# Kernel optimization log

Measured on AMD Instinct MI355X. Metric: run time of the kernel, lower is better.

The kernel has to match this reference:

```python
import jax, jax.numpy as jnp
import numpy as np

NEG = -1e30  # log-space 'zero' (avoid real -inf for stable exp/grad)


def _ctc_loss_mean(logp, targets, target_lengths, blank):
    """CTC loss, PyTorch semantics (reduction='mean', zero_infinity=True).
    logp: (B, T, V) log-probabilities; targets: (B, L) padded labels;
    target_lengths: (B,) ints. All input lengths are T (uniform here).
    """
    B, T, V = logp.shape
    L = targets.shape[1]
    S = 2 * L + 1  # extended label length: blank-interleaved

    ext = jnp.full((B, S), blank, dtype=targets.dtype)
    ext = ext.at[:, 1::2].set(targets)  # blanks at even s, labels at odd s

    s = jnp.arange(S)
    valid = s[None, :] < (2 * target_lengths + 1)[:, None]  # (B, S)
    prev2 = jnp.pad(ext[:, :-2], ((0, 0), (2, 0)), constant_values=blank)
    # skip transition s-2 -> s allowed only at non-blank s with no label repeat
    allow_skip = (s[None, :] >= 2) & (ext != blank) & (ext != prev2)

    # per-(t, s) emission log-prob, masked outside valid extended labels
    emit = jnp.take_along_axis(
        logp, jnp.broadcast_to(ext[:, None, :], (B, T, S)), axis=2
    )  # (B, T, S)
    emit = jnp.where(valid[:, None, :], emit, NEG)

    alpha0 = jnp.full((B, S), NEG, dtype=logp.dtype)
    alpha0 = alpha0.at[:, 0].set(emit[:, 0, 0])
    alpha0 = alpha0.at[:, 1].set(emit[:, 0, 1])

    def step(alpha, e):
        a1 = alpha
        a2 = jnp.pad(alpha[:, :-1], ((0, 0), (1, 0)), constant_values=NEG)
        a3 = jnp.pad(alpha[:, :-2], ((0, 0), (2, 0)), constant_values=NEG)
        a3 = jnp.where(allow_skip, a3, NEG)
        m = jnp.maximum(jnp.maximum(a1, a2), a3)
        new = m + jnp.log(jnp.exp(a1 - m) + jnp.exp(a2 - m) + jnp.exp(a3 - m)) + e
        return new, None

    alpha, _ = jax.lax.scan(step, alpha0, jnp.swapaxes(emit, 0, 1)[1:])

    i1 = (2 * target_lengths).astype(jnp.int32)
    l1 = jnp.take_along_axis(alpha, i1[:, None], axis=1)[:, 0]
    l2 = jnp.take_along_axis(alpha, jnp.maximum(i1 - 1, 0)[:, None], axis=1)[:, 0]
    l2 = jnp.where(target_lengths > 0, l2, NEG)
    m = jnp.maximum(l1, l2)
    loss = -(m + jnp.log(jnp.exp(l1 - m) + jnp.exp(l2 - m)))  # (B,)
    loss = jnp.where(loss > 1e20, 0.0, loss)  # zero_infinity=True
    # reduction='mean': divide by target length, then batch mean
    return jnp.mean(loss / jnp.maximum(target_lengths, 1).astype(loss.dtype))


def setup_inputs() -> dict:
    key = jax.random.key(0)
    kl, kt, kn = jax.random.split(key, 3)
    B, T, V, L = 32, 1024, 1000, 256
    logits = jax.random.normal(kl, (B, T, V), dtype=jnp.float32)
    targets = jax.random.randint(kt, (B, L), 1, V).astype(jnp.int32)
    lengths = jax.random.randint(kn, (B,), L // 2 + 2, L + 1)
    target_padding_mask = jnp.arange(L)[None, :] < lengths[:, None]  # bool (B, L)
    return {"logits": logits, "targets": targets,
            "target_padding_mask": target_padding_mask}


def reference(logits, targets, target_padding_mask):
    blank = 0
    lg = logits[:, :-1, :]            # drop last frame
    tgt = targets[:, 1:]              # drop leading (SOS) token
    logp = jax.nn.log_softmax(lg, axis=-1)  # (B, T-1, V)
    tlen = target_padding_mask.sum(axis=1).astype(jnp.int32) - 1
    return _ctc_loss_mean(logp, tgt, tlen, blank)
```

## Files before the change

### kernel.cpp

```cpp
#include <hip/hip_runtime.h>

#define LOG2E 1.4426950408889634f
#define LN2   0.6931471805599453

static constexpr int B  = 32;
static constexpr int T  = 1024;
static constexpr int TT = 1023;
static constexpr int V  = 1000;
static constexpr int L  = 256;
static constexpr int S  = 511;
static constexpr int SP = 512;
static constexpr int TP = 1024;

using h8  = __attribute__((ext_vector_type(8))) _Float16;

__device__ __forceinline__ float fexp2(float x) {
#if __has_builtin(__builtin_amdgcn_exp2f)
  return __builtin_amdgcn_exp2f(x);
#else
  return exp2f(x);
#endif
}
__device__ __forceinline__ float flog2(float x) {
#if __has_builtin(__builtin_amdgcn_logf)
  return __builtin_amdgcn_logf(x);
#else
  return log2f(x);
#endif
}

#if __has_builtin(__builtin_amdgcn_update_dpp)
#define HAVE_DPP 1
__device__ __forceinline__ float shr1f(float x) {
  int r = __builtin_amdgcn_update_dpp(0, __float_as_int(x), 0x138, 0xf, 0xf, true);
  return __int_as_float(r);
}
#define DPP_SWITCH(T, OLD, SRC, BC)                                            \
  T r;                                                                         \
  switch (ctrl) {                                                              \
    case 0x111: r = __builtin_amdgcn_update_dpp(OLD, SRC, 0x111, 0xf, 0xf, BC); break; \
    case 0x112: r = __builtin_amdgcn_update_dpp(OLD, SRC, 0x112, 0xf, 0xf, BC); break; \
    case 0x114: r = __builtin_amdgcn_update_dpp(OLD, SRC, 0x114, 0xf, 0xf, BC); break; \
    case 0x118: r = __builtin_amdgcn_update_dpp(OLD, SRC, 0x118, 0xf, 0xf, BC); break; \
    case 0x142: r = __builtin_amdgcn_update_dpp(OLD, SRC, 0x142, 0xf, 0xf, BC); break; \
    default:    r = __builtin_amdgcn_update_dpp(OLD, SRC, 0x143, 0xf, 0xf, BC); break; \
  }

__device__ __forceinline__ int dppmax_step(int m, const int ctrl) {
  DPP_SWITCH(int, 0, m, true);
  return max(m, r);
}
__device__ __forceinline__ int wavemax_to_sgpr(int m) {
  m = dppmax_step(m, 0x111);
  m = dppmax_step(m, 0x112);
  m = dppmax_step(m, 0x114);
  m = dppmax_step(m, 0x118);
  m = dppmax_step(m, 0x142);
  m = dppmax_step(m, 0x143);
  return __builtin_amdgcn_readlane(m, 63);
}
__device__ __forceinline__ float dppfmax_step(float x, const int ctrl) {
  int xi = __float_as_int(x);
  DPP_SWITCH(int, xi, xi, false);
  return fmaxf(x, __int_as_float(r));
}
__device__ __forceinline__ float wavefmax(float x) {
  x = dppfmax_step(x, 0x111);
  x = dppfmax_step(x, 0x112);
  x = dppfmax_step(x, 0x114);
  x = dppfmax_step(x, 0x118);
  x = dppfmax_step(x, 0x142);
  x = dppfmax_step(x, 0x143);
  return __int_as_float(__builtin_amdgcn_readlane(__float_as_int(x), 63));
}
__device__ __forceinline__ float dppfadd_step(float x, const int ctrl) {
  DPP_SWITCH(int, 0, __float_as_int(x), true);
  return x + __int_as_float(r);
}
__device__ __forceinline__ float wavefsum(float x) {
  x = dppfadd_step(x, 0x111);
  x = dppfadd_step(x, 0x112);
  x = dppfadd_step(x, 0x114);
  x = dppfadd_step(x, 0x118);
  x = dppfadd_step(x, 0x142);
  x = dppfadd_step(x, 0x143);
  return __int_as_float(__builtin_amdgcn_readlane(__float_as_int(x), 63));
}
#else
#define HAVE_DPP 0
__device__ __forceinline__ float shr1f(float x) {
  float r = __shfl_up(x, 1, 64);
  return (threadIdx.x & 63) == 0 ? 0.0f : r;
}
__device__ __forceinline__ int wavemax_to_sgpr(int m) {
  for (int o = 32; o >= 1; o >>= 1) m = max(m, __shfl_xor(m, o, 64));
  return m;
}
__device__ __forceinline__ float wavefmax(float x) {
  for (int o = 32; o >= 1; o >>= 1) x = fmaxf(x, __shfl_xor(x, o, 64));
  return x;
}
__device__ __forceinline__ float wavefsum(float x) {
  for (int o = 32; o >= 1; o >>= 1) x += __shfl_xor(x, o, 64);
  return x;
}
#endif

__global__ void k_tlen(const unsigned char* __restrict__ maskb,
                       int* __restrict__ tlen) {
  int b = blockIdx.x;
  int lane = threadIdx.x;
  int ca = 0;
  for (int k = lane; k < L; k += 64) ca += (maskb[b * L + k] != 0) ? 1 : 0;
  for (int o = 32; o >= 1; o >>= 1) ca += __shfl_xor(ca, o, 64);
  int cnt = ca;
  if (ca < 130) {
    const int* mi = (const int*)maskb;
    int cb = 0;
    for (int k = lane; k < L; k += 64) cb += (mi[b * L + k] != 0) ? 1 : 0;
    for (int o = 32; o >= 1; o >>= 1) cb += __shfl_xor(cb, o, 64);
    cnt = cb;
  }
  if (lane == 0) tlen[b] = cnt - 1;
}

__global__ __launch_bounds__(256) void k_emit(const float* __restrict__ logits,
                                              const int* __restrict__ targets,
                                              const int* __restrict__ tlenp,
                                              _Float16* __restrict__ E,
                                              float* __restrict__ G) {
  __shared__ float yrow[4][1024];
  const int wid = threadIdx.x >> 6;
  const int lane = threadIdx.x & 63;
  const int r = blockIdx.x * 4 + wid;
  const int b = r / TT;
  const int t = r - b * TT;

  const float4* row = reinterpret_cast<const float4*>(logits + ((size_t)b * T + t) * V);
  float* yw = yrow[wid];

  float4 u0 = row[lane];
  float4 u1 = row[lane + 64];
  float4 u2 = row[lane + 128];
  const bool has3 = (lane < 58);
  float4 u3 = has3 ? row[lane + 192]
                   : make_float4(-2.0e30f, -2.0e30f, -2.0e30f, -2.0e30f);

  u0.x *= LOG2E; u0.y *= LOG2E; u0.z *= LOG2E; u0.w *= LOG2E;
  u1.x *= LOG2E; u1.y *= LOG2E; u1.z *= LOG2E; u1.w *= LOG2E;
  u2.x *= LOG2E; u2.y *= LOG2E; u2.z *= LOG2E; u2.w *= LOG2E;
  u3.x *= LOG2E; u3.y *= LOG2E; u3.z *= LOG2E; u3.w *= LOG2E;

  reinterpret_cast<float4*>(yw)[lane]       = u0;
  reinterpret_cast<float4*>(yw)[lane + 64]  = u1;
  reinterpret_cast<float4*>(yw)[lane + 128] = u2;
  if (has3) reinterpret_cast<float4*>(yw)[lane + 192] = u3;

  float lm = fmaxf(fmaxf(fmaxf(u0.x, u0.y), fmaxf(u0.z, u0.w)),
                   fmaxf(fmaxf(u1.x, u1.y), fmaxf(u1.z, u1.w)));
  lm = fmaxf(lm, fmaxf(fmaxf(u2.x, u2.y), fmaxf(u2.z, u2.w)));
  lm = fmaxf(lm, fmaxf(fmaxf(u3.x, u3.y), fmaxf(u3.z, u3.w)));
  const float my = wavefmax(lm);

  float ps = fexp2(u0.x - my) + fexp2(u0.y - my) + fexp2(u0.z - my) + fexp2(u0.w - my)
           + fexp2(u1.x - my) + fexp2(u1.y - my) + fexp2(u1.z - my) + fexp2(u1.w - my)
           + fexp2(u2.x - my) + fexp2(u2.y - my) + fexp2(u2.z - my) + fexp2(u2.w - my)
           + fexp2(u3.x - my) + fexp2(u3.y - my) + fexp2(u3.z - my) + fexp2(u3.w - my);
  const float sum = wavefsum(ps);
  const float g = -flog2(sum);

  const int tl = tlenp[b];
  const int smax = 2 * tl + 1;
  const int base = b * L + (lane << 2);
  const int l1 = targets[base + 1];
  const int l2 = targets[base + 2];
  const int l3 = targets[base + 3];
  const int l4 = (lane == 63) ? 0 : targets[base + 4];
  const float yb = yw[0];
  const float eb = fexp2(yb - my);
  const float e1 = fexp2(yw[l1] - my);
  const float e2 = fexp2(yw[l2] - my);
  const float e3 = fexp2(yw[l3] - my);
  const float e4 = fexp2(yw[l4] - my);
  const int sb = lane << 3;
  h8 o;
  o[0] = (_Float16)((sb     < smax) ? eb : 0.0f);
  o[1] = (_Float16)((sb + 1 < smax) ? e1 : 0.0f);
  o[2] = (_Float16)((sb + 2 < smax) ? eb : 0.0f);
  o[3] = (_Float16)((sb + 3 < smax) ? e2 : 0.0f);
  o[4] = (_Float16)((sb + 4 < smax) ? eb : 0.0f);
  o[5] = (_Float16)((sb + 5 < smax) ? e3 : 0.0f);
  o[6] = (_Float16)((sb + 6 < smax) ? eb : 0.0f);
  o[7] = (_Float16)((lane < 63 && sb + 7 < smax) ? e4 : 0.0f);
  reinterpret_cast<h8*>(E + ((size_t)b * TP + t) * SP)[lane] = o;
  if (lane == 0) G[b * TT + t] = g;
}

__global__ __launch_bounds__(64, 1) void k_ctc(const _Float16* __restrict__ E,
                                               const int* __restrict__ targets,
                                               const int* __restrict__ tlenp,
                                               const float* __restrict__ G,
                                               float* __restrict__ lossb) {
  const int b = blockIdx.x;
  const int lane = threadIdx.x;
  const int s0 = lane << 3;
  const int* tg = targets + b * L;

  const int tl = tlenp[b];

  double gs = 0.0;
  for (int k = lane; k < TT; k += 64) gs += (double)G[b * TT + k];
  for (int o = 32; o >= 1; o >>= 1) gs += __shfl_xor(gs, o, 64);

  float f1 = 0.0f, f3, f5, f7 = 0.0f;
  {
    int s = s0 + 1;
    if (s >= 3) f1 = (tg[(s + 1) >> 1] != tg[(s - 1) >> 1]) ? 1.0f : 0.0f;
    s = s0 + 3;
    f3 = (tg[(s + 1) >> 1] != tg[(s - 1) >> 1]) ? 1.0f : 0.0f;
    s = s0 + 5;
    f5 = (tg[(s + 1) >> 1] != tg[(s - 1) >> 1]) ? 1.0f : 0.0f;
    s = s0 + 7;
    if (s < S) f7 = (tg[(s + 1) >> 1] != tg[(s - 1) >> 1]) ? 1.0f : 0.0f;
  }

  const _Float16* E0 = E + (size_t)b * TP * SP;
  const _Float16* Ebase = E0 + s0;

  float a0 = (lane == 0) ? (float)E0[0] : 0.0f;
  float a1 = (lane == 0) ? (float)E0[1] : 0.0f;
  float a2 = 0.f, a3 = 0.f, a4 = 0.f, a5 = 0.f, a6 = 0.f, a7 = 0.f;
  float n7 = 0.0f;
  int lsacc = 0;

  asm volatile("" :: "v"(f1), "v"(f3), "v"(f5), "v"(f7),
                     "v"(a0), "v"(a1), "v"(gs), "v"((float)tl));

#define GLROW4(d0, d1, d2, d3, p)                                \
  asm volatile("global_load_dwordx4 %0, %4, off\n\t"             \
               "global_load_dwordx4 %1, %4, off offset:1024\n\t" \
               "global_load_dwordx4 %2, %4, off offset:2048\n\t" \
               "global_load_dwordx4 %3, %4, off offset:3072"     \
               : "=&v"(d0), "=&v"(d1), "=&v"(d2), "=&v"(d3) : "v"(p))

#define LOAD8(P, r0)                                             \
  do {                                                           \
    const _Float16* q_ = Ebase + (size_t)(r0) * SP;              \
    GLROW4(P##0, P##1, P##2, P##3, q_);                          \
    GLROW4(P##4, P##5, P##6, P##7, q_ + 4 * SP);                 \
  } while (0)

#define VMWAIT8(n, P)                                            \
  do {                                                           \
    asm volatile("s_waitcnt vmcnt(" #n ")"                       \
                 : "+v"(P##0), "+v"(P##1), "+v"(P##2), "+v"(P##3), \
                   "+v"(P##4), "+v"(P##5), "+v"(P##6), "+v"(P##7)); \
    __builtin_amdgcn_sched_barrier(0);                           \
  } while (0)

#define STEPF(H)                                                \
  do {                                                          \
    float e7 = (float)(H)[7];                                   \
    float t7 = fmaf(f7, a5, a6 + a7) * e7;                      \
    float n7n = shr1f(t7);                                      \
    float e0 = (float)(H)[0], e1 = (float)(H)[1];               \
    float e2 = (float)(H)[2], e3 = (float)(H)[3];               \
    float e4 = (float)(H)[4], e5 = (float)(H)[5];               \
    float e6 = (float)(H)[6];                                   \
    float t0 = (a0 + n7) * e0;                                  \
    float t1 = fmaf(f1, n7, a0 + a1) * e1;                      \
    float t2 = (a1 + a2) * e2;                                  \
    float t3 = fmaf(f3, a1, a2 + a3) * e3;                      \
    float t4 = (a3 + a4) * e4;                                  \
    float t5 = fmaf(f5, a3, a4 + a5) * e5;                      \
    float t6 = (a5 + a6) * e6;                                  \
    a0 = t0; a1 = t1; a2 = t2; a3 = t3;                         \
    a4 = t4; a5 = t5; a6 = t6; a7 = t7;                         \
    n7 = n7n;                                                   \
  } while (0)

#define RESCALE()                                               \
  do {                                                          \
    int m = max(max(max(__float_as_int(a0), __float_as_int(a1)),\
                    max(__float_as_int(a2), __float_as_int(a3))),\
                max(max(__float_as_int(a4), __float_as_int(a5)),\
                    max(__float_as_int(a6), __float_as_int(a7))));\
    int mw = wavemax_to_sgpr(m);                                \
    int e = mw >> 23;                                           \
    int sh = 229 - e;                                           \
    lsacc += e - 229;                                           \
    a0 = ldexpf(a0, sh); a1 = ldexpf(a1, sh);                   \
    a2 = ldexpf(a2, sh); a3 = ldexpf(a3, sh);                   \
    a4 = ldexpf(a4, sh); a5 = ldexpf(a5, sh);                   \
    a6 = ldexpf(a6, sh); a7 = ldexpf(a7, sh);                   \
    n7 = ldexpf(n7, sh);                                        \
  } while (0)

#define PROC8R(P)                                               \
  do {                                                          \
    RESCALE();                                                  \
    STEPF(P##0); STEPF(P##1); STEPF(P##2); STEPF(P##3);         \
    STEPF(P##4); STEPF(P##5); STEPF(P##6); STEPF(P##7);         \
  } while (0)

  h8 A0, A1, A2, A3, A4, A5, A6, A7;
  h8 B0, B1, B2, B3, B4, B5, B6, B7;
  h8 C0, C1, C2, C3, C4, C5, C6, C7;
  h8 D0, D1, D2, D3, D4, D5, D6, D7;

  LOAD8(A, 1);
  LOAD8(B, 9);
  LOAD8(C, 17);
  LOAD8(D, 25);

  int t = 1;
#pragma unroll 1
  for (int it = 0; it < 30; ++it) {
    VMWAIT8(24, A); PROC8R(A); LOAD8(A, t + 32);
    VMWAIT8(24, B); PROC8R(B); LOAD8(B, t + 40);
    VMWAIT8(24, C); PROC8R(C); LOAD8(C, t + 48);
    VMWAIT8(24, D); PROC8R(D); LOAD8(D, t + 56);
    t += 32;
  }
  VMWAIT8(24, A); PROC8R(A); LOAD8(A, 993);
  VMWAIT8(24, B); PROC8R(B); LOAD8(B, 1001);
  VMWAIT8(24, C); PROC8R(C); LOAD8(C, 1009);
  VMWAIT8(24, D); PROC8R(D); LOAD8(D, 1017);
  VMWAIT8(24, A); PROC8R(A);
  VMWAIT8(16, B); PROC8R(B);
  VMWAIT8(8,  C); PROC8R(C);
  VMWAIT8(0,  D);
  RESCALE();
  STEPF(D0); STEPF(D1); STEPF(D2);
  STEPF(D3); STEPF(D4); STEPF(D5);
#undef GLROW4
#undef LOAD8
#undef VMWAIT8
#undef STEPF
#undef RESCALE
#undef PROC8R

  __shared__ float sal[SP];
  sal[s0 + 0] = a0; sal[s0 + 1] = a1; sal[s0 + 2] = a2; sal[s0 + 3] = a3;
  sal[s0 + 4] = a4; sal[s0 + 5] = a5; sal[s0 + 6] = a6; sal[s0 + 7] = a7;
  __syncthreads();
  if (lane == 0) {
    int i1 = 2 * tl;
    float p = sal[i1] + sal[(i1 > 0 ? i1 : 1) - 1];
    int hi = __float_as_int(p);
    int ep = (hi >> 23) - 127;
    float pm = ldexpf(p, -ep);
    float lm = flog2(pm);
    double loss2 = -((double)lm + (double)ep + (double)lsacc + gs);
    float loss = (float)(loss2 * LN2);
    if (!(loss <= 1e20f)) loss = 0.0f;
    int dv = (tl > 0) ? tl : 1;
    lossb[b] = loss / (float)dv;
  }
}

__global__ void k_mean(const float* __restrict__ lossb, float* __restrict__ out) {
  int lane = threadIdx.x;
  float v = (lane < B) ? lossb[lane] : 0.0f;
  for (int o = 32; o >= 1; o >>= 1) v += __shfl_xor(v, o, 64);
  if (lane == 0) out[0] = v / (float)B;
}

extern "C" void kernel_launch(void* const* d_in, const int* in_sizes, int n_in,
                              void* d_out, int out_size, void* d_ws, size_t ws_size,
                              hipStream_t stream) {
  const float* logits = (const float*)d_in[0];
  const int* targets = (const int*)d_in[1];
  const unsigned char* mask = (const unsigned char*)d_in[2];

  char* ws = (char*)d_ws;
  int* tlen = (int*)ws;
  float* lossb = (float*)(ws + 128);
  float* G = (float*)(ws + 512);
  _Float16* E = (_Float16*)(ws + 512 + 132 * 1024);

  k_tlen<<<B, 64, 0, stream>>>(mask, tlen);
  k_emit<<<(B * TT) / 4, 256, 0, stream>>>(logits, targets, tlen, E, G);
  k_ctc<<<B, 64, 0, stream>>>(E, targets, tlen, G, lossb);
  k_mean<<<1, 64, 0, stream>>>(lossb, (float*)d_out);
}
```

Before: 99.26 us.

## Software-pipeline emit kernel over four rows per wave with inline-asm loads

Each wave of the emission kernel now handles four rows instead of one. Inline-assembly global loads for up to three rows are issued ahead, and explicit vmcnt waits allow the next row's loads to be in flight while the current row is processed. Target labels are fetched as a single vector load, and the fourth label comes from the neighbouring lane via a DPP shift instead of a separate load. The grid shrinks by a factor of four, trading wave-level parallelism for memory-level parallelism inside each wave, with hand-tuned waitcnt values that are fragile.

After: 99.98 us. No clear change (+0.7%).

```diff
diff --git a/kernel.cpp b/kernel.cpp
--- a/kernel.cpp
+++ b/kernel.cpp
@@ -13,6 +13,8 @@
 static constexpr int TP = 1024;
 
 using h8  = __attribute__((ext_vector_type(8))) _Float16;
+using f4  = __attribute__((ext_vector_type(4))) float;
+using i4  = __attribute__((ext_vector_type(4))) int;
 
 __device__ __forceinline__ float fexp2(float x) {
 #if __has_builtin(__builtin_amdgcn_exp2f)
@@ -30,10 +32,12 @@
 }
 
 #if __has_builtin(__builtin_amdgcn_update_dpp)
-#define HAVE_DPP 1
 __device__ __forceinline__ float shr1f(float x) {
   int r = __builtin_amdgcn_update_dpp(0, __float_as_int(x), 0x138, 0xf, 0xf, true);
   return __int_as_float(r);
+}
+__device__ __forceinline__ int shl1i(int x) {
+  return __builtin_amdgcn_update_dpp(0, x, 0x130, 0xf, 0xf, true);
 }
 #define DPP_SWITCH(T, OLD, SRC, BC)                                            \
   T r;                                                                         \
@@ -87,10 +91,13 @@
   return __int_as_float(__builtin_amdgcn_readlane(__float_as_int(x), 63));
 }
 #else
-#define HAVE_DPP 0
 __device__ __forceinline__ float shr1f(float x) {
   float r = __shfl_up(x, 1, 64);
   return (threadIdx.x & 63) == 0 ? 0.0f : r;
+}
+__device__ __forceinline__ int shl1i(int x) {
+  int r = __shfl_down(x, 1, 64);
+  return (threadIdx.x & 63) == 63 ? 0 : r;
 }
 __device__ __forceinline__ int wavemax_to_sgpr(int m) {
   for (int o = 32; o >= 1; o >>= 1) m = max(m, __shfl_xor(m, o, 64));
@@ -124,76 +131,105 @@
   if (lane == 0) tlen[b] = cnt - 1;
 }
 
-__global__ __launch_bounds__(256) void k_emit(const float* __restrict__ logits,
-                                              const int* __restrict__ targets,
-                                              const int* __restrict__ tlenp,
-                                              _Float16* __restrict__ E,
-                                              float* __restrict__ G) {
+__global__ __launch_bounds__(256, 4) void k_emit(const float* __restrict__ logits,
+                                                 const int* __restrict__ targets,
+                                                 const int* __restrict__ tlenp,
+                                                 _Float16* __restrict__ E,
+                                                 float* __restrict__ G) {
   __shared__ float yrow[4][1024];
   const int wid = threadIdx.x >> 6;
   const int lane = threadIdx.x & 63;
-  const int r = blockIdx.x * 4 + wid;
-  const int b = r / TT;
-  const int t = r - b * TT;
-
-  const float4* row = reinterpret_cast<const float4*>(logits + ((size_t)b * T + t) * V);
   float* yw = yrow[wid];
-
-  float4 u0 = row[lane];
-  float4 u1 = row[lane + 64];
-  float4 u2 = row[lane + 128];
-  const bool has3 = (lane < 58);
-  float4 u3 = has3 ? row[lane + 192]
-                   : make_float4(-2.0e30f, -2.0e30f, -2.0e30f, -2.0e30f);
-
-  u0.x *= LOG2E; u0.y *= LOG2E; u0.z *= LOG2E; u0.w *= LOG2E;
-  u1.x *= LOG2E; u1.y *= LOG2E; u1.z *= LOG2E; u1.w *= LOG2E;
-  u2.x *= LOG2E; u2.y *= LOG2E; u2.z *= LOG2E; u2.w *= LOG2E;
-  u3.x *= LOG2E; u3.y *= LOG2E; u3.z *= LOG2E; u3.w *= LOG2E;
-
-  reinterpret_cast<float4*>(yw)[lane]       = u0;
-  reinterpret_cast<float4*>(yw)[lane + 64]  = u1;
-  reinterpret_cast<float4*>(yw)[lane + 128] = u2;
-  if (has3) reinterpret_cast<float4*>(yw)[lane + 192] = u3;
-
-  float lm = fmaxf(fmaxf(fmaxf(u0.x, u0.y), fmaxf(u0.z, u0.w)),
-                   fmaxf(fmaxf(u1.x, u1.y), fmaxf(u1.z, u1.w)));
-  lm = fmaxf(lm, fmaxf(fmaxf(u2.x, u2.y), fmaxf(u2.z, u2.w)));
-  lm = fmaxf(lm, fmaxf(fmaxf(u3.x, u3.y), fmaxf(u3.z, u3.w)));
-  const float my = wavefmax(lm);
-
-  float ps = fexp2(u0.x - my) + fexp2(u0.y - my) + fexp2(u0.z - my) + fexp2(u0.w - my)
-           + fexp2(u1.x - my) + fexp2(u1.y - my) + fexp2(u1.z - my) + fexp2(u1.w - my)
-           + fexp2(u2.x - my) + fexp2(u2.y - my) + fexp2(u2.z - my) + fexp2(u2.w - my)
-           + fexp2(u3.x - my) + fexp2(u3.y - my) + fexp2(u3.z - my) + fexp2(u3.w - my);
-  const float sum = wavefsum(ps);
-  const float g = -flog2(sum);
-
-  const int tl = tlenp[b];
-  const int smax = 2 * tl + 1;
-  const int base = b * L + (lane << 2);
-  const int l1 = targets[base + 1];
-  const int l2 = targets[base + 2];
-  const int l3 = targets[base + 3];
-  const int l4 = (lane == 63) ? 0 : targets[base + 4];
-  const float yb = yw[0];
-  const float eb = fexp2(yb - my);
-  const float e1 = fexp2(yw[l1] - my);
-  const float e2 = fexp2(yw[l2] - my);
-  const float e3 = fexp2(yw[l3] - my);
-  const float e4 = fexp2(yw[l4] - my);
+  const int w0 = blockIdx.x * 4 + wid;
   const int sb = lane << 3;
-  h8 o;
-  o[0] = (_Float16)((sb     < smax) ? eb : 0.0f);
-  o[1] = (_Float16)((sb + 1 < smax) ? e1 : 0.0f);
-  o[2] = (_Float16)((sb + 2 < smax) ? eb : 0.0f);
-  o[3] = (_Float16)((sb + 3 < smax) ? e2 : 0.0f);
-  o[4] = (_Float16)((sb + 4 < smax) ? eb : 0.0f);
-  o[5] = (_Float16)((sb + 5 < smax) ? e3 : 0.0f);
-  o[6] = (_Float16)((sb + 6 < smax) ? eb : 0.0f);
-  o[7] = (_Float16)((lane < 63 && sb + 7 < smax) ? e4 : 0.0f);
-  reinterpret_cast<h8*>(E + ((size_t)b * TP + t) * SP)[lane] = o;
-  if (lane == 0) G[b * TT + t] = g;
+
+#define EISSUE(P, r)                                              \
+  do {                                                            \
+    int b_ = (r) / TT;                                            \
+    int t_ = (r) - b_ * TT;                                       \
+    const float* rp_ = logits + ((size_t)b_ * T + t_) * V + (lane << 2); \
+    const int* tp_ = targets + b_ * L + (lane << 2);              \
+    const int* lp_ = tlenp + b_;                                  \
+    asm volatile(                                                 \
+      "global_load_dwordx4 %0, %6, off\n\t"                       \
+      "global_load_dwordx4 %1, %6, off offset:1024\n\t"           \
+      "global_load_dwordx4 %2, %6, off offset:2048\n\t"           \
+      "global_load_dwordx4 %3, %6, off offset:3072\n\t"           \
+      "global_load_dwordx4 %4, %7, off\n\t"                       \
+      "global_load_dword %5, %8, off"                             \
+      : "=&v"(P##u0), "=&v"(P##u1), "=&v"(P##u2), "=&v"(P##u3),   \
+        "=&v"(P##tv), "=&v"(P##tl)                                \
+      : "v"(rp_), "v"(tp_), "v"(lp_));                            \
+  } while (0)
+
+#define EWAIT(n, P)                                               \
+  do {                                                            \
+    asm volatile("s_waitcnt vmcnt(" #n ")"                        \
+                 : "+v"(P##u0), "+v"(P##u1), "+v"(P##u2),         \
+                   "+v"(P##u3), "+v"(P##tv), "+v"(P##tl));        \
+    __builtin_amdgcn_sched_barrier(0);                            \
+  } while (0)
+
+#define EPROC(P, r)                                               \
+  do {                                                            \
+    int b_ = (r) / TT;                                            \
+    int t_ = (r) - b_ * TT;                                       \
+    f4 v0 = P##u0 * LOG2E;                                        \
+    f4 v1 = P##u1 * LOG2E;                                        \
+    f4 v2 = P##u2 * LOG2E;                                        \
+    f4 v3 = P##u3 * LOG2E;                                        \
+    const bool has3 = (lane < 58);         \
+    if (!has3) { v3[0] = v3[1] = v3[2] = v3[3] = -2.0e30f; }      \
+    reinterpret_cast<f4*>(yw)[lane]       = v0;                   \
+    reinterpret_cast<f4*>(yw)[lane + 64]  = v1;                   \
+    reinterpret_cast<f4*>(yw)[lane + 128] = v2;                   \
+    if (has3) reinterpret_cast<f4*>(yw)[lane + 192] = v3;         \
+    float lm = fmaxf(fmaxf(fmaxf(v0[0], v0[1]), fmaxf(v0[2], v0[3])), \
+                     fmaxf(fmaxf(v1[0], v1[1]), fmaxf(v1[2], v1[3]))); \
+    lm = fmaxf(lm, fmaxf(fmaxf(v2[0], v2[1]), fmaxf(v2[2], v2[3]))); \
+    lm = fmaxf(lm, fmaxf(fmaxf(v3[0], v3[1]), fmaxf(v3[2], v3[3]))); \
+    const float my = wavefmax(lm);                                \
+    float ps = fexp2(v0[0]-my) + fexp2(v0[1]-my) + fexp2(v0[2]-my) + fexp2(v0[3]-my) \
+             + fexp2(v1[0]-my) + fexp2(v1[1]-my) + fexp2(v1[2]-my) + fexp2(v1[3]-my) \
+             + fexp2(v2[0]-my) + fexp2(v2[1]-my) + fexp2(v2[2]-my) + fexp2(v2[3]-my) \
+             + fexp2(v3[0]-my) + fexp2(v3[1]-my) + fexp2(v3[2]-my) + fexp2(v3[3]-my); \
+    const float g = -flog2(wavefsum(ps));                         \
+    const int smax = 2 * P##tl + 1;                               \
+    const int l1 = P##tv[1], l2 = P##tv[2], l3 = P##tv[3];        \
+    const int l4 = shl1i(P##tv[0]);              \
+    const float eb = fexp2(yw[0]  - my);                          \
+    const float e1 = fexp2(yw[l1] - my);                          \
+    const float e2 = fexp2(yw[l2] - my);                          \
+    const float e3 = fexp2(yw[l3] - my);                          \
+    const float e4 = fexp2(yw[l4] - my);                          \
+    h8 o;                                                         \
+    o[0] = (_Float16)((sb     < smax) ? eb : 0.0f);               \
+    o[1] = (_Float16)((sb + 1 < smax) ? e1 : 0.0f);               \
+    o[2] = (_Float16)((sb + 2 < smax) ? eb : 0.0f);               \
+    o[3] = (_Float16)((sb + 3 < smax) ? e2 : 0.0f);               \
+    o[4] = (_Float16)((sb + 4 < smax) ? eb : 0.0f);               \
+    o[5] = (_Float16)((sb + 5 < smax) ? e3 : 0.0f);               \
+    o[6] = (_Float16)((sb + 6 < smax) ? eb : 0.0f);               \
+    o[7] = (_Float16)((lane < 63 && sb + 7 < smax) ? e4 : 0.0f);  \
+    reinterpret_cast<h8*>(E + ((size_t)b_ * TP + t_) * SP)[lane] = o; \
+    if (lane == 0) G[r] = g;                                      \
+  } while (0)
+
+  f4 Au0, Au1, Au2, Au3; i4 Atv; int Atl;
+  f4 Bu0, Bu1, Bu2, Bu3; i4 Btv; int Btl;
+  f4 Cu0, Cu1, Cu2, Cu3; i4 Ctv; int Ctl;
+
+  EISSUE(A, w0);
+  EISSUE(B, w0 + 8184);
+  EISSUE(C, w0 + 16368);
+  EWAIT(12, A); EPROC(A, w0);
+  EISSUE(A, w0 + 24552);
+  EWAIT(12, B); EPROC(B, w0 + 8184);
+  EWAIT(6,  C); EPROC(C, w0 + 16368);
+  EWAIT(0,  A); EPROC(A, w0 + 24552);
+#undef EISSUE
+#undef EWAIT
+#undef EPROC
 }
 
 __global__ __launch_bounds__(64, 1) void k_ctc(const _Float16* __restrict__ E,
@@ -380,7 +416,7 @@
   _Float16* E = (_Float16*)(ws + 512 + 132 * 1024);
 
   k_tlen<<<B, 64, 0, stream>>>(mask, tlen);
-  k_emit<<<(B * TT) / 4, 256, 0, stream>>>(logits, targets, tlen, E, G);
+  k_emit<<<(B * TT) / 16, 256, 0, stream>>>(logits, targets, tlen, E, G);
   k_ctc<<<B, 64, 0, stream>>>(E, targets, tlen, G, lossb);
   k_mean<<<1, 64, 0, stream>>>(lossb, (float*)d_out);
 }
```
